# Kernel tuning notes

Hardware: AMD Instinct MI355X
Metric: run time of the kernel (lower is better)

Reference implementation:

```python
import jax, jax.numpy as jnp
import numpy as np

B = 262144  # batch of joint configurations (original module processes one at a time)


def setup_inputs() -> dict:
    key = jax.random.key(0)
    k = jax.random.split(key, 7)
    joints = jax.random.normal(k[0], (B, 7), dtype=jnp.float32)
    # fk_params rows: (alpha, a, d, theta_offset) per joint
    fk_params = jax.random.normal(k[1], (7, 4), dtype=jnp.float32) * 0.5
    # nn.Linear(7,15), nn.Linear(15,15), nn.Linear(15,7): y = x @ W.T + b
    W1 = jax.random.normal(k[2], (15, 7), dtype=jnp.float32) * 0.3
    b1 = jax.random.normal(k[3], (15,), dtype=jnp.float32) * 0.1
    W2 = jax.random.normal(k[4], (15, 15), dtype=jnp.float32) * 0.3
    b2 = jax.random.normal(k[5], (15,), dtype=jnp.float32) * 0.1
    W3 = jax.random.normal(k[6], (7, 15), dtype=jnp.float32) * 0.3
    b3 = jnp.zeros((7,), dtype=jnp.float32)
    return {"joints": joints, "fk_params": fk_params,
            "W1": W1, "b1": b1, "W2": W2, "b2": b2, "W3": W3, "b3": b3}


def reference(joints, fk_params, W1, b1, W2, b2, W3, b3):
    # 7-15-15-7 tanh MLP correction
    h = jnp.tanh(joints @ W1.T + b1)
    h = jnp.tanh(h @ W2.T + b2)
    correction = jnp.tanh(h @ W3.T + b3)
    theta = joints + correction                         # [B,7]

    alpha = fk_params[:, 0]                             # [7]
    a = fk_params[:, 1]
    d = fk_params[:, 2]
    offset = fk_params[:, 3]

    th = theta + offset                                 # [B,7]
    ct, st = jnp.cos(th), jnp.sin(th)                   # [B,7]
    ca, sa = jnp.cos(alpha), jnp.sin(alpha)             # [7]
    z = jnp.zeros_like(ct)
    o = jnp.ones_like(ct)

    # DH transform per (batch, joint): [B,7,4,4]
    row0 = jnp.stack([ct,      -st,       z,       a * o      ], axis=-1)
    row1 = jnp.stack([st * ca,  ct * ca, -sa * o, -d * sa * o ], axis=-1)
    row2 = jnp.stack([st * sa,  ct * sa,  ca * o,  ca * d * o ], axis=-1)
    row3 = jnp.stack([z,        z,        z,       o          ], axis=-1)
    M = jnp.stack([row0, row1, row2, row3], axis=-2)    # [B,7,4,4]

    # serial chain multiply over the 7 joints (fixed, small loop)
    ee = M[:, 0]
    for j in range(1, 7):
        ee = ee @ M[:, j]

    # wrist_transform[:-1, -1] -> translation part
    return ee[:, :3, 3]                                 # [B,3]
```

## Files before the change

kernel.cpp:

```cpp
#include <hip/hip_runtime.h>
#include <math.h>

#define BLK 256

__device__ __forceinline__ float fast_tanh(float x) {
    x = fminf(9.0f, fmaxf(-9.0f, x));
    float e = __expf(2.0f * x);
    return fmaf(-2.0f, __frcp_rn(e + 1.0f), 1.0f);
}

__device__ __forceinline__ void fast_sincos(float x, float& s, float& c) {
    const float INV2PI = 0.15915494309189535f;
    float r = x * INV2PI;
    r = r - floorf(r);
    s = __builtin_amdgcn_sinf(r);
    c = __builtin_amdgcn_cosf(r);
}

__global__ __launch_bounds__(BLK) void fk_fused_kernel(
    const float* __restrict__ joints,
    const float* __restrict__ fk_params,
    const float* __restrict__ W1, const float* __restrict__ b1,
    const float* __restrict__ W2, const float* __restrict__ b2,
    const float* __restrict__ W3, const float* __restrict__ b3,
    float* __restrict__ out,
    int B)
{
    __shared__ float sJ[BLK * 7];

    const int t = threadIdx.x;
    const int base = blockIdx.x * BLK;

    const int nval = min(BLK * 7, B * 7 - base * 7);
    for (int i = t; i < nval; i += BLK) sJ[i] = joints[base * 7 + i];
    __syncthreads();

    const int sample = base + t;
    float r0[4], r1[4], r2[4];

    if (sample < B) {
        float j[7];
        #pragma unroll
        for (int k = 0; k < 7; ++k) j[k] = sJ[t * 7 + k];

        float h1[15];
        #pragma unroll
        for (int i = 0; i < 15; ++i) {
            float s = b1[i];
            #pragma unroll
            for (int k = 0; k < 7; ++k) s = fmaf(j[k], W1[i * 7 + k], s);
            h1[i] = fast_tanh(s);
        }
        float h2[15];
        #pragma unroll
        for (int i = 0; i < 15; ++i) {
            float s = b2[i];
            #pragma unroll
            for (int k = 0; k < 15; ++k) s = fmaf(h1[k], W2[i * 15 + k], s);
            h2[i] = fast_tanh(s);
        }

        #pragma unroll
        for (int jj = 0; jj < 7; ++jj) {
            float s = b3[jj];
            #pragma unroll
            for (int k = 0; k < 15; ++k) s = fmaf(h2[k], W3[jj * 15 + k], s);
            float corr = fast_tanh(s);

            const float alpha = fk_params[jj * 4 + 0];
            const float a     = fk_params[jj * 4 + 1];
            const float d     = fk_params[jj * 4 + 2];
            const float off   = fk_params[jj * 4 + 3];

            float th = j[jj] + corr + off;
            float st, ct, sa, ca;
            fast_sincos(th, st, ct);
            fast_sincos(alpha, sa, ca);

            const float m10 = st * ca, m11 = ct * ca, m12 = -sa, m13 = -d * sa;
            const float m20 = st * sa, m21 = ct * sa, m22 = ca,  m23 = ca * d;
            if (jj == 0) {
                r0[0] = ct;  r0[1] = -st; r0[2] = 0.0f; r0[3] = a;
                r1[0] = m10; r1[1] = m11; r1[2] = m12;  r1[3] = m13;
                r2[0] = m20; r2[1] = m21; r2[2] = m22;  r2[3] = m23;
            } else {
                float n0, n1, n2, n3;
                n0 = r0[0]*ct + r0[1]*m10 + r0[2]*m20;
                n1 = -r0[0]*st + r0[1]*m11 + r0[2]*m21;
                n2 =             r0[1]*m12 + r0[2]*m22;
                n3 = r0[0]*a  + r0[1]*m13 + r0[2]*m23 + r0[3];
                r0[0]=n0; r0[1]=n1; r0[2]=n2; r0[3]=n3;
                n0 = r1[0]*ct + r1[1]*m10 + r1[2]*m20;
                n1 = -r1[0]*st + r1[1]*m11 + r1[2]*m21;
                n2 =             r1[1]*m12 + r1[2]*m22;
                n3 = r1[0]*a  + r1[1]*m13 + r1[2]*m23 + r1[3];
                r1[0]=n0; r1[1]=n1; r1[2]=n2; r1[3]=n3;
                n0 = r2[0]*ct + r2[1]*m10 + r2[2]*m20;
                n1 = -r2[0]*st + r2[1]*m11 + r2[2]*m21;
                n2 =             r2[1]*m12 + r2[2]*m22;
                n3 = r2[0]*a  + r2[1]*m13 + r2[2]*m23 + r2[3];
                r2[0]=n0; r2[1]=n1; r2[2]=n2; r2[3]=n3;
            }
        }
    }

    __syncthreads();
    if (sample < B) {
        sJ[t * 3 + 0] = r0[3];
        sJ[t * 3 + 1] = r1[3];
        sJ[t * 3 + 2] = r2[3];
    }
    __syncthreads();
    const int onval = min(BLK * 3, B * 3 - base * 3);
    for (int i = t; i < onval; i += BLK) out[base * 3 + i] = sJ[i];
}

extern "C" void kernel_launch(void* const* d_in, const int* in_sizes, int n_in,
                              void* d_out, int out_size, void* d_ws, size_t ws_size,
                              hipStream_t stream) {
    const float* joints    = (const float*)d_in[0];
    const float* fk_params = (const float*)d_in[1];
    const float* W1 = (const float*)d_in[2];
    const float* b1 = (const float*)d_in[3];
    const float* W2 = (const float*)d_in[4];
    const float* b2 = (const float*)d_in[5];
    const float* W3 = (const float*)d_in[6];
    const float* b3 = (const float*)d_in[7];
    float* out = (float*)d_out;

    const int B = in_sizes[0] / 7;
    const int nblk = (B + BLK - 1) / BLK;
    fk_fused_kernel<<<nblk, BLK, 0, stream>>>(joints, fk_params, W1, b1, W2, b2,
                                              W3, b3, out, B);
}
```

Baseline: 83.66 us.

## Pack weights into padded workspace and process two samples per thread

Adds a one-block pack kernel that copies the MLP weights into a 16-float-aligned workspace and precomputes sin/cos of the DH alpha terms, so the main kernel can read weights as float4 and skips the per-sample alpha trig. The main kernel handles two samples per thread to reuse each weight load, and uses float4 LDS staging for input and output on full blocks. This costs an extra launch and more registers per thread. The layer-3 loop also holds a dead, overwritten partial accumulation that the compiler should drop.

```diff
diff --git a/kernel.cpp b/kernel.cpp
--- a/kernel.cpp
+++ b/kernel.cpp
@@ -2,6 +2,17 @@
 #include <math.h>
 
 #define BLK 256
+#define SPT 2
+#define SPB (BLK * SPT)
+
+#define OFF_W1 0
+#define OFF_W2 128
+#define OFF_W3 384
+#define OFF_B1 512
+#define OFF_B2 528
+#define OFF_B3 544
+#define OFF_FK 560
+#define WS_FLOATS 616
 
 __device__ __forceinline__ float fast_tanh(float x) {
     x = fminf(9.0f, fmaxf(-9.0f, x));
@@ -17,102 +28,176 @@
     c = __builtin_amdgcn_cosf(r);
 }
 
-__global__ __launch_bounds__(BLK) void fk_fused_kernel(
-    const float* __restrict__ joints,
-    const float* __restrict__ fk_params,
-    const float* __restrict__ W1, const float* __restrict__ b1,
-    const float* __restrict__ W2, const float* __restrict__ b2,
-    const float* __restrict__ W3, const float* __restrict__ b3,
-    float* __restrict__ out,
-    int B)
+__global__ __launch_bounds__(BLK) void pack_kernel(
+    const float* __restrict__ fk, const float* __restrict__ W1,
+    const float* __restrict__ b1, const float* __restrict__ W2,
+    const float* __restrict__ b2, const float* __restrict__ W3,
+    const float* __restrict__ b3, float* __restrict__ ws)
 {
-    __shared__ float sJ[BLK * 7];
-
     const int t = threadIdx.x;
-    const int base = blockIdx.x * BLK;
-
-    const int nval = min(BLK * 7, B * 7 - base * 7);
-    for (int i = t; i < nval; i += BLK) sJ[i] = joints[base * 7 + i];
-    __syncthreads();
-
-    const int sample = base + t;
-    float r0[4], r1[4], r2[4];
-
-    if (sample < B) {
-        float j[7];
-        #pragma unroll
-        for (int k = 0; k < 7; ++k) j[k] = sJ[t * 7 + k];
-
-        float h1[15];
-        #pragma unroll
-        for (int i = 0; i < 15; ++i) {
-            float s = b1[i];
-            #pragma unroll
-            for (int k = 0; k < 7; ++k) s = fmaf(j[k], W1[i * 7 + k], s);
-            h1[i] = fast_tanh(s);
-        }
-        float h2[15];
-        #pragma unroll
-        for (int i = 0; i < 15; ++i) {
-            float s = b2[i];
-            #pragma unroll
-            for (int k = 0; k < 15; ++k) s = fmaf(h1[k], W2[i * 15 + k], s);
-            h2[i] = fast_tanh(s);
-        }
-
-        #pragma unroll
-        for (int jj = 0; jj < 7; ++jj) {
-            float s = b3[jj];
-            #pragma unroll
-            for (int k = 0; k < 15; ++k) s = fmaf(h2[k], W3[jj * 15 + k], s);
-            float corr = fast_tanh(s);
-
-            const float alpha = fk_params[jj * 4 + 0];
-            const float a     = fk_params[jj * 4 + 1];
-            const float d     = fk_params[jj * 4 + 2];
-            const float off   = fk_params[jj * 4 + 3];
-
-            float th = j[jj] + corr + off;
-            float st, ct, sa, ca;
+    for (int i = t; i < WS_FLOATS; i += BLK) ws[i] = 0.0f;
+    __syncthreads();
+    for (int i = t; i < 120; i += BLK) { int r = i >> 3, c = i & 7;  if (c < 7)  ws[OFF_W1 + i] = W1[r * 7  + c]; }
+    for (int i = t; i < 240; i += BLK) { int r = i >> 4, c = i & 15; if (c < 15) ws[OFF_W2 + i] = W2[r * 15 + c]; }
+    for (int i = t; i < 112; i += BLK) { int r = i >> 4, c = i & 15; if (c < 15) ws[OFF_W3 + i] = W3[r * 15 + c]; }
+    if (t < 15) { ws[OFF_B1 + t] = b1[t]; ws[OFF_B2 + t] = b2[t]; }
+    if (t < 7) {
+        ws[OFF_B3 + t] = b3[t];
+        float al = fk[4 * t], a = fk[4 * t + 1], d = fk[4 * t + 2], off = fk[4 * t + 3];
+        float sa = sinf(al), ca = cosf(al);
+        float* p = ws + OFF_FK + 8 * t;
+        p[0] = ca; p[1] = sa; p[2] = a; p[3] = d; p[4] = off;
+        p[5] = d * sa; p[6] = d * ca; p[7] = 0.0f;
+    }
+}
+
+__global__ __launch_bounds__(BLK) void fk_main(
+    const float* __restrict__ joints, const float* __restrict__ wsf,
+    float* __restrict__ out, int B)
+{
+    const float4* __restrict__ w4 = (const float4*)wsf;
+    __shared__ float sJ[SPB * 7];
+    const int t = threadIdx.x;
+    const int base = blockIdx.x * SPB;
+    const int rem = B - base;
+
+    if (rem >= SPB) {
+        const float4* gsrc = (const float4*)(joints + base * 7);
+        float4* ldst = (float4*)sJ;
+        #pragma unroll
+        for (int i = 0; i < (SPB * 7) / (4 * BLK); ++i) ldst[t + i * BLK] = gsrc[t + i * BLK];
+        { int i = ((SPB * 7) / (4 * BLK)) * BLK + t; if (i < (SPB * 7) / 4) ldst[i] = gsrc[i]; }
+    } else {
+        const int nval = rem * 7;
+        for (int i = t; i < nval; i += BLK) sJ[i] = joints[base * 7 + i];
+    }
+    __syncthreads();
+
+    float j[SPT][7];
+    float r[SPT][3][4];
+    bool valid[SPT];
+
+    #pragma unroll
+    for (int s = 0; s < SPT; ++s) {
+        const int ss = t + s * BLK;
+        valid[s] = (base + ss) < B;
+        #pragma unroll
+        for (int k = 0; k < 7; ++k) j[s][k] = valid[s] ? sJ[ss * 7 + k] : 0.0f;
+    }
+
+    float h1[SPT][15];
+    #pragma unroll
+    for (int i = 0; i < 15; ++i) {
+        const float4 wa = w4[(OFF_W1 >> 2) + 2 * i];
+        const float4 wb = w4[(OFF_W1 >> 2) + 2 * i + 1];
+        const float bi = wsf[OFF_B1 + i];
+        #pragma unroll
+        for (int s = 0; s < SPT; ++s) {
+            float a0 = bi;
+            a0 = fmaf(j[s][0], wa.x, a0); a0 = fmaf(j[s][1], wa.y, a0);
+            a0 = fmaf(j[s][2], wa.z, a0); a0 = fmaf(j[s][3], wa.w, a0);
+            a0 = fmaf(j[s][4], wb.x, a0); a0 = fmaf(j[s][5], wb.y, a0);
+            a0 = fmaf(j[s][6], wb.z, a0);
+            h1[s][i] = fast_tanh(a0);
+        }
+    }
+    float h2[SPT][15];
+    #pragma unroll
+    for (int i = 0; i < 15; ++i) {
+        const float4 wa = w4[(OFF_W2 >> 2) + 4 * i + 0];
+        const float4 wb = w4[(OFF_W2 >> 2) + 4 * i + 1];
+        const float4 wc = w4[(OFF_W2 >> 2) + 4 * i + 2];
+        const float4 wd = w4[(OFF_W2 >> 2) + 4 * i + 3];
+        const float bi = wsf[OFF_B2 + i];
+        #pragma unroll
+        for (int s = 0; s < SPT; ++s) {
+            float a0 = bi;
+            a0 = fmaf(h1[s][0],  wa.x, a0); a0 = fmaf(h1[s][1],  wa.y, a0);
+            a0 = fmaf(h1[s][2],  wa.z, a0); a0 = fmaf(h1[s][3],  wa.w, a0);
+            a0 = fmaf(h1[s][4],  wb.x, a0); a0 = fmaf(h1[s][5],  wb.y, a0);
+            a0 = fmaf(h1[s][6],  wb.z, a0); a0 = fmaf(h1[s][7],  wb.w, a0);
+            a0 = fmaf(h1[s][8],  wc.x, a0); a0 = fmaf(h1[s][9],  wc.y, a0);
+            a0 = fmaf(h1[s][10], wc.z, a0); a0 = fmaf(h1[s][11], wc.w, a0);
+            a0 = fmaf(h1[s][12], wd.x, a0); a0 = fmaf(h1[s][13], wd.y, a0);
+            a0 = fmaf(h1[s][14], wd.z, a0);
+            h2[s][i] = fast_tanh(a0);
+        }
+    }
+    #pragma unroll
+    for (int jj = 0; jj < 7; ++jj) {
+        const float4 wa = w4[(OFF_W3 >> 2) + 4 * jj + 0];
+        const float4 wb = w4[(OFF_W3 >> 2) + 4 * jj + 1];
+        const float4 wc = w4[(OFF_W3 >> 2) + 4 * jj + 2];
+        const float4 wd = w4[(OFF_W3 >> 2) + 4 * jj + 3];
+        const float bi  = wsf[OFF_B3 + jj];
+        const float ca  = wsf[OFF_FK + 8 * jj + 0];
+        const float sa  = wsf[OFF_FK + 8 * jj + 1];
+        const float a   = wsf[OFF_FK + 8 * jj + 2];
+        const float off = wsf[OFF_FK + 8 * jj + 4];
+        const float dsa = wsf[OFF_FK + 8 * jj + 5];
+        const float dca = wsf[OFF_FK + 8 * jj + 6];
+        #pragma unroll
+        for (int s = 0; s < SPT; ++s) {
+            float a0 = bi;
+            a0 = fmaf(h2[s][0],  wa.x, a0); a0 = fmaf(h2[s][1],  wa.y, a0);
+            a0 = fmaf(h2[s][2],  wa.z, a0); a0 = fmaf(h2[s][3],  wa.w, a0);
+            a0 = fmaf(h2[s][4],  wb.x, a0); a0 = fmaf(h2[s][5],  wb.y, a0);
+            a0 = fmaf(h2[s][6],  wb.w == 0.0f ? wb.w : wb.w, a0);
+            a0 = fmaf(h2[s][6],  0.0f, a0);
+            a0 = a0;
+            a0 = bi;
+            a0 = fmaf(h2[s][0],  wa.x, a0); a0 = fmaf(h2[s][1],  wa.y, a0);
+            a0 = fmaf(h2[s][2],  wa.z, a0); a0 = fmaf(h2[s][3],  wa.w, a0);
+            a0 = fmaf(h2[s][4],  wb.x, a0); a0 = fmaf(h2[s][5],  wb.y, a0);
+            a0 = fmaf(h2[s][6],  wb.z, a0); a0 = fmaf(h2[s][7],  wb.w, a0);
+            a0 = fmaf(h2[s][8],  wc.x, a0); a0 = fmaf(h2[s][9],  wc.y, a0);
+            a0 = fmaf(h2[s][10], wc.z, a0); a0 = fmaf(h2[s][11], wc.w, a0);
+            a0 = fmaf(h2[s][12], wd.x, a0); a0 = fmaf(h2[s][13], wd.y, a0);
+            a0 = fmaf(h2[s][14], wd.z, a0);
+            const float corr = fast_tanh(a0);
+            const float th = j[s][jj] + corr + off;
+            float st, ct;
             fast_sincos(th, st, ct);
-            fast_sincos(alpha, sa, ca);
-
-            const float m10 = st * ca, m11 = ct * ca, m12 = -sa, m13 = -d * sa;
-            const float m20 = st * sa, m21 = ct * sa, m22 = ca,  m23 = ca * d;
+            const float m10 = st * ca, m11 = ct * ca;
+            const float m20 = st * sa, m21 = ct * sa;
             if (jj == 0) {
-                r0[0] = ct;  r0[1] = -st; r0[2] = 0.0f; r0[3] = a;
-                r1[0] = m10; r1[1] = m11; r1[2] = m12;  r1[3] = m13;
-                r2[0] = m20; r2[1] = m21; r2[2] = m22;  r2[3] = m23;
+                r[s][0][0] = ct;  r[s][0][1] = -st;  r[s][0][2] = 0.0f; r[s][0][3] = a;
+                r[s][1][0] = m10; r[s][1][1] = m11;  r[s][1][2] = -sa;  r[s][1][3] = -dsa;
+                r[s][2][0] = m20; r[s][2][1] = m21;  r[s][2][2] = ca;   r[s][2][3] = dca;
             } else {
-                float n0, n1, n2, n3;
-                n0 = r0[0]*ct + r0[1]*m10 + r0[2]*m20;
-                n1 = -r0[0]*st + r0[1]*m11 + r0[2]*m21;
-                n2 =             r0[1]*m12 + r0[2]*m22;
-                n3 = r0[0]*a  + r0[1]*m13 + r0[2]*m23 + r0[3];
-                r0[0]=n0; r0[1]=n1; r0[2]=n2; r0[3]=n3;
-                n0 = r1[0]*ct + r1[1]*m10 + r1[2]*m20;
-                n1 = -r1[0]*st + r1[1]*m11 + r1[2]*m21;
-                n2 =             r1[1]*m12 + r1[2]*m22;
-                n3 = r1[0]*a  + r1[1]*m13 + r1[2]*m23 + r1[3];
-                r1[0]=n0; r1[1]=n1; r1[2]=n2; r1[3]=n3;
-                n0 = r2[0]*ct + r2[1]*m10 + r2[2]*m20;
-                n1 = -r2[0]*st + r2[1]*m11 + r2[2]*m21;
-                n2 =             r2[1]*m12 + r2[2]*m22;
-                n3 = r2[0]*a  + r2[1]*m13 + r2[2]*m23 + r2[3];
-                r2[0]=n0; r2[1]=n1; r2[2]=n2; r2[3]=n3;
+                #pragma unroll
+                for (int i = 0; i < 3; ++i) {
+                    const float e0 = r[s][i][0], e1 = r[s][i][1], e2 = r[s][i][2], e3 = r[s][i][3];
+                    r[s][i][0] = e0 * ct + e1 * m10 + e2 * m20;
+                    r[s][i][1] = -e0 * st + e1 * m11 + e2 * m21;
+                    r[s][i][2] = e1 * -sa + e2 * ca;
+                    r[s][i][3] = e0 * a + e1 * -dsa + e2 * dca + e3;
+                }
             }
         }
     }
 
     __syncthreads();
-    if (sample < B) {
-        sJ[t * 3 + 0] = r0[3];
-        sJ[t * 3 + 1] = r1[3];
-        sJ[t * 3 + 2] = r2[3];
-    }
-    __syncthreads();
-    const int onval = min(BLK * 3, B * 3 - base * 3);
-    for (int i = t; i < onval; i += BLK) out[base * 3 + i] = sJ[i];
+    #pragma unroll
+    for (int s = 0; s < SPT; ++s) {
+        const int ss = t + s * BLK;
+        if (valid[s]) {
+            sJ[ss * 3 + 0] = r[s][0][3];
+            sJ[ss * 3 + 1] = r[s][1][3];
+            sJ[ss * 3 + 2] = r[s][2][3];
+        }
+    }
+    __syncthreads();
+    const int onval = min(SPB * 3, (B - base) * 3);
+    if (onval == SPB * 3) {
+        float4* gdst = (float4*)(out + base * 3);
+        const float4* lsrc = (const float4*)sJ;
+        #pragma unroll
+        for (int i = 0; i < (SPB * 3) / (4 * BLK); ++i) gdst[t + i * BLK] = lsrc[t + i * BLK];
+        { int i = ((SPB * 3) / (4 * BLK)) * BLK + t; if (i < (SPB * 3) / 4) gdst[i] = lsrc[i]; }
+    } else {
+        for (int i = t; i < onval; i += BLK) out[base * 3 + i] = sJ[i];
+    }
 }
 
 extern "C" void kernel_launch(void* const* d_in, const int* in_sizes, int n_in,
@@ -127,9 +212,10 @@
     const float* W3 = (const float*)d_in[6];
     const float* b3 = (const float*)d_in[7];
     float* out = (float*)d_out;
+    float* ws  = (float*)d_ws;
 
     const int B = in_sizes[0] / 7;
-    const int nblk = (B + BLK - 1) / BLK;
-    fk_fused_kernel<<<nblk, BLK, 0, stream>>>(joints, fk_params, W1, b1, W2, b2,
-                                              W3, b3, out, B);
-}
+    pack_kernel<<<1, BLK, 0, stream>>>(fk_params, W1, b1, W2, b2, W3, b3, ws);
+    const int nblk = (B + SPB - 1) / SPB;
+    fk_main<<<nblk, BLK, 0, stream>>>(joints, ws, out, B);
+}
```

After: 93.51 us. +11.8%, slower.
